# Kernel tuning notes

Measured on AMD Instinct MI355X. Metric: run time of the kernel, lower is better.

## Reference

```python
import jax, jax.numpy as jnp
import numpy as np

PATCH = 3  # patch_sizes[layer] == 3 for all layers
EPS_NORM = 1e-12   # F.normalize eps
EPS_DIV = 1e-8     # fold divisor eps


def _extract_patches(f, p):
    # F.unfold(kernel=p, stride=1, padding=p//2) -> (b, N=h*w, c, p, p)
    b, c, h, w = f.shape
    pad = p // 2
    xp = jnp.pad(f, ((0, 0), (0, 0), (pad, pad), (pad, pad)))
    # stack the p*p shifted views: (b, c, p*p, h, w)
    pats = jnp.stack([xp[:, :, i:i + h, j:j + w]
                      for i in range(p) for j in range(p)], axis=2)
    # -> (b, c, p, p, N) -> (b, N, c, p, p), matching unfold's (c, kh, kw) ordering
    return pats.reshape(b, c, p, p, h * w).transpose(0, 4, 1, 2, 3)


def _fold(patches, h, w, p):
    # F.fold inverse of unfold: scatter-add overlapping patches.
    # patches: (b, N=h*w, c, p, p)
    b, n, c = patches.shape[:3]
    pad = p // 2
    m = patches.reshape(b, h, w, c, p, p).transpose(0, 3, 4, 5, 1, 2)  # (b,c,p,p,h,w)
    out = jnp.zeros((b, c, h + 2 * pad, w + 2 * pad), patches.dtype)
    for ki in range(p):
        for kj in range(p):
            out = out.at[:, :, ki:ki + h, kj:kj + w].add(m[:, :, ki, kj])
    return out[:, :, pad:pad + h, pad:pad + w]


def _mrf_loss(content_feats, style_feats, p):
    b, c, h, w = content_feats.shape
    d = c * p * p
    cp = _extract_patches(content_feats, p)            # (b, N, c, p, p)
    sp = _extract_patches(style_feats, p)              # (b, M, c, p, p)
    cv = cp.reshape(b, -1, d)
    sv = sp.reshape(b, -1, d)
    cv = cv / jnp.maximum(jnp.linalg.norm(cv, axis=2, keepdims=True), EPS_NORM)
    svn = sv / jnp.maximum(jnp.linalg.norm(sv, axis=2, keepdims=True), EPS_NORM)
    # cosine similarity matrix (b, N, M) -- the big memory-bound intermediate
    dist = jnp.einsum('bnd,bmd->bnm', cv, svn)
    best = jnp.argmax(dist, axis=2)                    # (b, N) int
    # gather matched (un-normalized) style patches
    matched = jnp.take_along_axis(sp.reshape(b, -1, d), best[:, :, None], axis=1)
    matched = matched.reshape(b, -1, c, p, p)
    out = _fold(matched, h, w, p)
    ones = jnp.ones((1, h * w, 1, p, p), content_feats.dtype)
    divisor = _fold(ones, h, w, p)                      # overlap counts (1,1,h,w)
    recon = out / (divisor + EPS_DIV)
    return jnp.mean((content_feats - recon) ** 2)


def setup_inputs() -> dict:
    key = jax.random.key(0)
    k1, k2 = jax.random.split(key)
    content_feats = jax.random.normal(k1, (1, 128, 96, 96), dtype=jnp.float32)
    style_feats = jax.random.normal(k2, (1, 128, 96, 96), dtype=jnp.float32)
    return {"content_feats": content_feats, "style_feats": style_feats}


def reference(content_feats, style_feats):
    return _mrf_loss(content_feats, style_feats, PATCH)
```

## Files before the change

### kernel.cpp

```cpp
#include <hip/hip_runtime.h>
#include <hip/hip_bf16.h>

#define HH 96
#define WW 96
#define NPIX 9216
#define NCH 128
#define DDIM 1152
#define TOTAL_ELEMS 1179648
#define CG 32
#define DDIAG 9217
#define DROW 884832

typedef float f32x4 __attribute__((ext_vector_type(4)));
typedef __bf16 bf16x8 __attribute__((ext_vector_type(8)));
typedef _Float16 half8 __attribute__((ext_vector_type(8)));

__device__ __forceinline__ void gload_lds16(const void* g, void* l) {
  __builtin_amdgcn_global_load_lds((const __attribute__((address_space(1))) void*)g,
                                   (__attribute__((address_space(3))) void*)l, 16, 0, 0);
}


#define GUARD_ELEMS 894064ull
constexpr size_t G_CORE_ELEMS = (size_t)NPIX * NPIX;
constexpr size_t G_TOT_ELEMS = G_CORE_ELEMS + 2ull * GUARD_ELEMS;
constexpr size_t GBYTES = ((G_TOT_ELEMS * 2 + 255) & ~(size_t)255);
constexpr size_t CT_OFF = GBYTES;
constexpr size_t ST2_OFF = CT_OFF + (size_t)NPIX * NCH * 2;
constexpr size_t STYT_OFF = ST2_OFF + (size_t)NPIX * NCH * 2;
constexpr size_t SS_OFF = STYT_OFF + (size_t)NPIX * NCH * 4;
constexpr size_t RN2_OFF = SS_OFF + (size_t)NPIX * 4;
constexpr size_t KEY2_OFF = RN2_OFF + (size_t)NPIX * 4;
constexpr size_t NEED_NEW = KEY2_OFF + (size_t)NPIX * 8;

__global__ __launch_bounds__(256)
void transpose_kernel(const float* __restrict__ style_f, const float* __restrict__ content_f,
                      _Float16* __restrict__ St, _Float16* __restrict__ Ct,
                      float* __restrict__ styT, float* __restrict__ ss) {
  __shared__ float ftile[NCH][97];
  const int y = blockIdx.x;
  const bool is_style = (blockIdx.y == 0);
  const float* f = is_style ? style_f : content_f;
  _Float16* P = is_style ? St : Ct;
  const int tid = threadIdx.x;
  for (int i = tid; i < NCH * WW; i += 256) {
    int c = i / WW, x = i - (i / WW) * WW;
    ftile[c][x] = f[(size_t)c * NPIX + y * WW + x];
  }
  __syncthreads();
  for (int j = tid; j < WW * NCH; j += 256) {
    int x = j >> 7, c = j & 127;
    float v = ftile[c][x];
    P[(size_t)(y * WW + x) * NCH + c] = (_Float16)v;
    if (is_style) styT[(size_t)(y * WW + x) * NCH + c] = v;
  }
  if (is_style && tid < WW) {
    float s = 0.f;
#pragma unroll 8
    for (int c = 0; c < NCH; ++c) { float v = ftile[c][tid]; s = fmaf(v, v, s); }
    ss[y * WW + tid] = s;
  }
}

__global__ __launch_bounds__(256)
void boxnorm_kernel(const float* __restrict__ ss, float* __restrict__ rnorm) {
  int m = blockIdx.x * 256 + threadIdx.x;
  int ym = m / WW, xm = m - (m / WW) * WW;
  float s = 0.f;
#pragma unroll
  for (int di = -1; di <= 1; ++di) {
    int yy = ym + di;
    if (yy < 0 || yy >= HH) continue;
#pragma unroll
    for (int dj = -1; dj <= 1; ++dj) {
      int xx = xm + dj;
      if (xx < 0 || xx >= WW) continue;
      s += ss[yy * WW + xx];
    }
  }
  rnorm[m] = 1.0f / fmaxf(sqrtf(s), 1e-12f);
}

__global__ __launch_bounds__(256, 2)
void ggemm_kernel(const _Float16* __restrict__ Ct, const _Float16* __restrict__ St,
                  unsigned short* __restrict__ Gg) {
  __shared__ char smem[65536];
  const int tid = threadIdx.x;
  const int lane = tid & 63, wid = tid >> 6;
  const int l15 = lane & 15, lg = lane >> 4;
  const int wm = wid >> 1, wn = wid & 1;
  const int n0 = blockIdx.x * 128, m0 = blockIdx.y * 128;

  {
    const int r = tid >> 4, p = tid & 15;
    const int l = p ^ (r & 7);
    const _Float16* sa = Ct + (size_t)(n0 + r) * NCH + l * 8;
    const _Float16* sb = St + (size_t)(m0 + r) * NCH + l * 8;
    char* d = smem + tid * 16;
#pragma unroll
    for (int i = 0; i < 8; ++i) {
      gload_lds16(sa + (size_t)16 * i * NCH, d + 4096 * i);
      gload_lds16(sb + (size_t)16 * i * NCH, d + 32768 + 4096 * i);
    }
  }
  __syncthreads();

  f32x4 acc[4][4];
#pragma unroll
  for (int mf = 0; mf < 4; ++mf)
#pragma unroll
    for (int nf = 0; nf < 4; ++nf) {
      f32x4 z = {0.f, 0.f, 0.f, 0.f};
      acc[mf][nf] = z;
    }

#pragma unroll
  for (int ks = 0; ks < 4; ++ks) {
    half8 af[4], bb[4];
#pragma unroll
    for (int mf = 0; mf < 4; ++mf) {
      int row = wm * 64 + mf * 16 + l15;
      int phys = (ks * 4 + lg) ^ (row & 7);
      af[mf] = __builtin_bit_cast(half8, *(const int4*)(smem + row * 256 + phys * 16));
    }
#pragma unroll
    for (int nf = 0; nf < 4; ++nf) {
      int row = wn * 64 + nf * 16 + l15;
      int phys = (ks * 4 + lg) ^ (row & 7);
      bb[nf] = __builtin_bit_cast(half8, *(const int4*)(smem + 32768 + row * 256 + phys * 16));
    }
#pragma unroll
    for (int mf = 0; mf < 4; ++mf)
#pragma unroll
      for (int nf = 0; nf < 4; ++nf)
        acc[mf][nf] = __builtin_amdgcn_mfma_f32_16x16x32_f16(af[mf], bb[nf], acc[mf][nf], 0, 0, 0);
  }
  __syncthreads();

#pragma unroll
  for (int mf = 0; mf < 4; ++mf)
#pragma unroll
    for (int nf = 0; nf < 4; ++nf)
#pragma unroll
      for (int r = 0; r < 4; ++r) {
        int row = wm * 64 + mf * 16 + lg * 4 + r;
        int col = wn * 64 + nf * 16 + l15;
        *(_Float16*)(smem + (row * 136 + col) * 2) = (_Float16)acc[mf][nf][r];
      }
  __syncthreads();
  const size_t gbase = GUARD_ELEMS + (size_t)n0 * NPIX + m0;
#pragma unroll
  for (int j = 0; j < 8; ++j) {
    int idx = j * 256 + tid;
    int row = idx >> 4, ch = idx & 15;
    int4 v = *(const int4*)(smem + (row * 136 + ch * 8) * 2);
    *(int4*)(Gg + gbase + (size_t)row * NPIX + ch * 8) = v;
  }
}

__global__ __launch_bounds__(256)
void dist_argmax_kernel(const _Float16* __restrict__ Gg, const float* __restrict__ rnorm,
                        unsigned long long* __restrict__ keytab) {
  const int bid = blockIdx.x;
  const int xcd = bid & 7;
  const int local = bid >> 3;
  const int nt = xcd * 9 + (local % 9);
  const int rest = local / 9;
  const int ms = rest % 18;
  const int sh = rest / 18;
  const int w = threadIdx.x >> 6;
  const int lane = threadIdx.x & 63;
  const int n0 = nt * 128 + w * 32 + sh * 16;
  const int m8 = ms * 512 + lane * 8;

  const int ym = m8 / WW;
  const int x8 = m8 - ym * WW;
  const float me0 = (x8 == 0) ? 0.f : 1.f;
  const float me7 = (x8 == 88) ? 0.f : 1.f;
  const bool mr0 = (ym >= 1);
  const bool mr2 = (ym <= 94);
  float rnv[8];
  *(f32x4*)(rnv) = *(const f32x4*)(rnorm + m8);
  *(f32x4*)(rnv + 4) = *(const f32x4*)(rnorm + m8 + 4);

  const _Float16* base = Gg + ((size_t)n0 * NPIX + (size_t)m8 + GUARD_ELEMS);
  const _Float16* pL0 = base - DROW - DDIAG;
  const _Float16* pC0 = base - DROW;
  const _Float16* pR0 = base - DROW + DDIAG - 1;
  const _Float16* pL1 = base - DDIAG;
  const _Float16* pC1 = base;
  const _Float16* pR1 = base + DDIAG - 1;
  const _Float16* pL2 = base + DROW - DDIAG;
  const _Float16* pC2 = base + DROW;
  const _Float16* pR2 = base + DROW + DDIAG - 1;

  int yn = n0 / WW;
  int xn = n0 - yn * WW;

#pragma unroll 2
  for (int s = 0; s < 16; ++s) {
    const int n = n0 + s;
    const float cn0 = (xn >= 1) ? 1.f : 0.f;
    const float cn2 = (xn <= 94) ? 1.f : 0.f;
    const float rb0 = (mr0 && (yn >= 1)) ? 1.f : 0.f;
    const float rb2 = (mr2 && (yn <= 94)) ? 1.f : 0.f;
    float d[8];
    {
      half8 C = *(const half8*)pC1;
      _Float16 P = pL1[0];
      half8 L = *(const half8*)(pL1 + 1);
      half8 R = *(const half8*)pR1;
      _Float16 X = pR1[8];
#pragma unroll
      for (int j = 0; j < 8; ++j) d[j] = (float)C[j];
      d[0] = fmaf((float)P, cn0 * me0, d[0]);
#pragma unroll
      for (int j = 1; j < 8; ++j) d[j] = fmaf((float)L[j - 1], cn0, d[j]);
#pragma unroll
      for (int j = 0; j < 7; ++j) d[j] = fmaf((float)R[j + 1], cn2, d[j]);
      d[7] = fmaf((float)X, cn2 * me7, d[7]);
    }
    {
      const float wl = rb0 * cn0, wr = rb0 * cn2;
      half8 C = *(const half8*)pC0;
      _Float16 P = pL0[0];
      half8 L = *(const half8*)(pL0 + 1);
      half8 R = *(const half8*)pR0;
      _Float16 X = pR0[8];
#pragma unroll
      for (int j = 0; j < 8; ++j) d[j] = fmaf((float)C[j], rb0, d[j]);
      d[0] = fmaf((float)P, wl * me0, d[0]);
#pragma unroll
      for (int j = 1; j < 8; ++j) d[j] = fmaf((float)L[j - 1], wl, d[j]);
#pragma unroll
      for (int j = 0; j < 7; ++j) d[j] = fmaf((float)R[j + 1], wr, d[j]);
      d[7] = fmaf((float)X, wr * me7, d[7]);
    }
    {
      const float wl = rb2 * cn0, wr = rb2 * cn2;
      half8 C = *(const half8*)pC2;
      _Float16 P = pL2[0];
      half8 L = *(const half8*)(pL2 + 1);
      half8 R = *(const half8*)pR2;
      _Float16 X = pR2[8];
#pragma unroll
      for (int j = 0; j < 8; ++j) d[j] = fmaf((float)C[j], rb2, d[j]);
      d[0] = fmaf((float)P, wl * me0, d[0]);
#pragma unroll
      for (int j = 1; j < 8; ++j) d[j] = fmaf((float)L[j - 1], wl, d[j]);
#pragma unroll
      for (int j = 0; j < 7; ++j) d[j] = fmaf((float)R[j + 1], wr, d[j]);
      d[7] = fmaf((float)X, wr * me7, d[7]);
    }
    float bv = d[0] * rnv[0];
    int bj = m8;
#pragma unroll
    for (int j = 1; j < 8; ++j) {
      float xs = d[j] * rnv[j];
      if (xs > bv) { bv = xs; bj = m8 + j; }
    }
    float wmx = bv;
#pragma unroll
    for (int mm = 1; mm < 64; mm <<= 1)
      wmx = fmaxf(wmx, __shfl_xor(wmx, mm, 64));
    if (bv == wmx) {
      unsigned u = __float_as_uint(bv);
      u ^= (unsigned)((int)u >> 31) | 0x80000000u;
      unsigned long long key =
          ((unsigned long long)u << 32) | (unsigned)(0xFFFFFFFFu ^ (unsigned)bj);
      atomicMax(keytab + n, key);
    }
    pL0 += NPIX; pC0 += NPIX; pR0 += NPIX;
    pL1 += NPIX; pC1 += NPIX; pR1 += NPIX;
    pL2 += NPIX; pC2 += NPIX; pR2 += NPIX;
    ++xn;
    if (xn == WW) { xn = 0; ++yn; }
  }
}

__global__ __launch_bounds__(256)
void recon_mse2_kernel(const _Float16* __restrict__ Ct, const float* __restrict__ styT,
                       const unsigned long long* __restrict__ keytab, float* __restrict__ out) {
  const int pix = blockIdx.x * 2 + (threadIdx.x >> 7);
  const int c = threadIdx.x & 127;
  const int y = pix / WW, x = pix - (pix / WW) * WW;
  float sum = 0.f, cnt = 0.f;
#pragma unroll
  for (int ki = 0; ki < 3; ++ki) {
    int yn = y - ki + 1;
    if (yn < 0 || yn >= HH) continue;
#pragma unroll
    for (int kj = 0; kj < 3; ++kj) {
      int xn = x - kj + 1;
      if (xn < 0 || xn >= WW) continue;
      cnt += 1.f;
      int m = (int)(0xFFFFFFFFu ^ (unsigned)(keytab[yn * WW + xn] & 0xFFFFFFFFull));
      int ys = m / WW, xs = m - (m / WW) * WW;
      int sy = ys + ki - 1, sx = xs + kj - 1;
      if (sy >= 0 && sy < HH && sx >= 0 && sx < WW)
        sum += styT[(size_t)(sy * WW + sx) * NCH + c];
    }
  }
  float recon = sum / (cnt + 1e-8f);
  float cv = (float)Ct[(size_t)pix * NCH + c];
  float diff = cv - recon;
  float sq = diff * diff;
#pragma unroll
  for (int m = 32; m > 0; m >>= 1) sq += __shfl_down(sq, m, 64);
  __shared__ float wsum[4];
  int lane = threadIdx.x & 63, w = threadIdx.x >> 6;
  if (lane == 0) wsum[w] = sq;
  __syncthreads();
  if (threadIdx.x == 0)
    atomicAdd(out, (wsum[0] + wsum[1] + wsum[2] + wsum[3]) * (1.0f / (float)TOTAL_ELEMS));
}

__global__ __launch_bounds__(256)
void build_patches_old(const float* __restrict__ style_f, const float* __restrict__ content_f,
                       __bf16* __restrict__ Ps, __bf16* __restrict__ Pc) {
  __shared__ float ftile[CG][3][104];
  const int y = blockIdx.x;
  const int cg = blockIdx.y;
  const bool is_style = (blockIdx.z == 0);
  const float* f = is_style ? style_f : content_f;
  __bf16* P = is_style ? Ps : Pc;
  const int tid = threadIdx.x;
  for (int i = tid; i < CG * 3 * 96; i += 256) {
    int cl = i / 288, rem = i - cl * 288;
    int yy = rem / 96, xx = rem - yy * 96;
    int gy = y + yy - 1;
    float v = (gy >= 0 && gy < HH) ? f[(size_t)(cg * CG + cl) * NPIX + gy * WW + xx] : 0.f;
    ftile[cl][yy][xx] = v;
  }
  __syncthreads();
  for (int j = tid; j < 96 * 36; j += 256) {
    int px = j / 36, wi = j - px * 36;
    bf16x8 tmp;
#pragma unroll
    for (int u = 0; u < 8; ++u) {
      int e = wi * 8 + u;
      int cl = e / 9, t = e - cl * 9;
      int ki = t / 3, kj = t - ki * 3;
      int xx = px + kj - 1;
      float v = (xx >= 0 && xx < WW) ? ftile[cl][ki][xx] : 0.f;
      tmp[u] = (__bf16)v;
    }
    *(bf16x8*)(P + (size_t)(y * WW + px) * DDIM + cg * 288 + wi * 8) = tmp;
  }
}

__global__ __launch_bounds__(256)
void norm_old(const __bf16* __restrict__ Ps, float* __restrict__ rnorm) {
  const int n = blockIdx.x * 4 + (threadIdx.x >> 6);
  const int lane = threadIdx.x & 63;
  const bf16x8* row = (const bf16x8*)(Ps + (size_t)n * DDIM);
  float ss = 0.f;
#pragma unroll
  for (int i = 0; i < 3; ++i) {
    int idx = i * 64 + lane;
    if (idx < 144) {
      bf16x8 v = row[idx];
#pragma unroll
      for (int u = 0; u < 8; ++u) { float x = (float)v[u]; ss += x * x; }
    }
  }
#pragma unroll
  for (int m = 1; m < 64; m <<= 1) ss += __shfl_xor(ss, m, 64);
  if (lane == 0) rnorm[n] = 1.0f / fmaxf(sqrtf(ss), 1e-12f);
}

__global__ __launch_bounds__(256, 2)
void gemm_old(const __bf16* __restrict__ Pc, const __bf16* __restrict__ Ps,
              const float* __restrict__ rnorm, unsigned long long* __restrict__ keytab) {
  __shared__ int4 smem4[4608];
  char* smem = (char*)smem4;
  const int tid = threadIdx.x;
  const int lane = tid & 63;
  const int wid = tid >> 6;
  const int l15 = lane & 15;
  const int lg = lane >> 4;
  const int wm = wid >> 1;
  const int wn = wid & 1;
  const int orig = blockIdx.x;
  const int swz = (orig & 7) * 324 + (orig >> 3);
  const int mt = swz / 72;
  const int nt = swz - mt * 72;
  const int bm0 = mt * 256;
  const int sbase = nt * 128;
  const int srow = tid >> 2;
  const int sg = (tid & 3) ^ ((srow >> 1) & 3);
  const __bf16* pa = Pc + (size_t)(bm0 + srow) * DDIM + sg * 8;
  const __bf16* pb = Ps + (size_t)(sbase + srow) * DDIM + sg * 8;
  const int sdst = tid * 16;
  auto stage = [&](int buf, int kt) {
    char* la = smem + buf * 24576 + sdst;
    const int ko = kt * 32;
#pragma unroll
    for (int i = 0; i < 4; ++i) gload_lds16(pa + (size_t)i * 64 * DDIM + ko, la + i * 4096);
#pragma unroll
    for (int j = 0; j < 2; ++j) gload_lds16(pb + (size_t)j * 64 * DDIM + ko, la + 16384 + j * 4096);
  };
  const int sx = (lg ^ ((l15 >> 1) & 3)) << 4;
  int aoff[8], boff[4];
#pragma unroll
  for (int mf = 0; mf < 8; ++mf) aoff[mf] = (wm * 128 + mf * 16 + l15) * 64 + sx;
#pragma unroll
  for (int nf = 0; nf < 4; ++nf) boff[nf] = 16384 + (wn * 64 + nf * 16 + l15) * 64 + sx;
  f32x4 acc[8][4];
#pragma unroll
  for (int mf = 0; mf < 8; ++mf)
#pragma unroll
    for (int nf = 0; nf < 4; ++nf) {
      f32x4 z = {0.f, 0.f, 0.f, 0.f};
      acc[mf][nf] = z;
    }
  auto compute = [&](int buf) {
    const char* bp = smem + buf * 24576;
    bf16x8 af[8], bfr[4];
#pragma unroll
    for (int mf = 0; mf < 8; ++mf) af[mf] = __builtin_bit_cast(bf16x8, *(const int4*)(bp + aoff[mf]));
#pragma unroll
    for (int nf = 0; nf < 4; ++nf) bfr[nf] = __builtin_bit_cast(bf16x8, *(const int4*)(bp + boff[nf]));
    __builtin_amdgcn_s_setprio(1);
#pragma unroll
    for (int mf = 0; mf < 8; ++mf)
#pragma unroll
      for (int nf = 0; nf < 4; ++nf)
        acc[mf][nf] = __builtin_amdgcn_mfma_f32_16x16x32_bf16(af[mf], bfr[nf], acc[mf][nf], 0, 0, 0);
    __builtin_amdgcn_s_setprio(0);
  };
  stage(0, 0);
  stage(1, 1);
  int sb = 2, cb = 0;
  for (int kt = 0; kt < 34; ++kt) {
    stage(sb, kt + 2);
    sb = (sb == 2) ? 0 : sb + 1;
    asm volatile("s_waitcnt vmcnt(12)" ::: "memory");
    __builtin_amdgcn_s_barrier();
    __builtin_amdgcn_sched_barrier(0);
    compute(cb);
    __builtin_amdgcn_s_barrier();
    cb = (cb == 2) ? 0 : cb + 1;
  }
  asm volatile("s_waitcnt vmcnt(6)" ::: "memory");
  __builtin_amdgcn_s_barrier();
  __builtin_amdgcn_sched_barrier(0);
  compute(cb);
  cb = (cb == 2) ? 0 : cb + 1;
  asm volatile("s_waitcnt vmcnt(0)" ::: "memory");
  __builtin_amdgcn_s_barrier();
  __builtin_amdgcn_sched_barrier(0);
  compute(cb);
  float rn[4];
#pragma unroll
  for (int nf = 0; nf < 4; ++nf) rn[nf] = rnorm[sbase + wn * 64 + nf * 16 + l15];
#pragma unroll
  for (int mf = 0; mf < 8; ++mf)
#pragma unroll
    for (int r = 0; r < 4; ++r) {
      float v = -3.0e38f;
      int bi = 0;
#pragma unroll
      for (int nf = 0; nf < 4; ++nf) {
        float x = acc[mf][nf][r] * rn[nf];
        int col = sbase + wn * 64 + nf * 16 + l15;
        if (x > v) { v = x; bi = col; }
      }
#pragma unroll
      for (int m = 1; m < 16; m <<= 1) {
        float ov = __shfl_xor(v, m, 64);
        int oi = __shfl_xor(bi, m, 64);
        if (ov > v || (ov == v && oi < bi)) { v = ov; bi = oi; }
      }
      if (l15 == 0) {
        int row = bm0 + wm * 128 + mf * 16 + lg * 4 + r;
        unsigned u = __float_as_uint(v);
        u ^= (unsigned)((int)u >> 31) | 0x80000000u;
        unsigned long long key = ((unsigned long long)u << 32) | (unsigned)(0xFFFFFFFFu ^ (unsigned)bi);
        atomicMax(keytab + row, key);
      }
    }
}

__global__ __launch_bounds__(256)
void recon_old(const __bf16* __restrict__ Pc, const __bf16* __restrict__ Ps,
               const unsigned long long* __restrict__ keytab, float* __restrict__ out) {
  const int pix = blockIdx.x * 2 + (threadIdx.x >> 7);
  const int c = threadIdx.x & 127;
  const int y = pix / WW, x = pix - (pix / WW) * WW;
  float sum = 0.f, cnt = 0.f;
#pragma unroll
  for (int ki = 0; ki < 3; ++ki) {
    int yn = y - ki + 1;
    if (yn < 0 || yn >= HH) continue;
#pragma unroll
    for (int kj = 0; kj < 3; ++kj) {
      int xn = x - kj + 1;
      if (xn < 0 || xn >= WW) continue;
      cnt += 1.f;
      int m = (int)(0xFFFFFFFFu ^ (unsigned)(keytab[yn * WW + xn] & 0xFFFFFFFFull));
      sum += (float)Ps[(size_t)m * DDIM + c * 9 + ki * 3 + kj];
    }
  }
  float recon = sum / (cnt + 1e-8f);
  float cv = (float)Pc[(size_t)pix * DDIM + c * 9 + 4];
  float diff = cv - recon;
  float sq = diff * diff;
#pragma unroll
  for (int m = 32; m > 0; m >>= 1) sq += __shfl_down(sq, m, 64);
  __shared__ float wsum[4];
  int lane = threadIdx.x & 63, w = threadIdx.x >> 6;
  if (lane == 0) wsum[w] = sq;
  __syncthreads();
  if (threadIdx.x == 0)
    atomicAdd(out, (wsum[0] + wsum[1] + wsum[2] + wsum[3]) * (1.0f / (float)TOTAL_ELEMS));
}

extern "C" void kernel_launch(void* const* d_in, const int* in_sizes, int n_in,
                              void* d_out, int out_size, void* d_ws, size_t ws_size,
                              hipStream_t stream) {
  const float* content = (const float*)d_in[0];
  const float* stylef = (const float*)d_in[1];
  float* out = (float*)d_out;
  char* ws = (char*)d_ws;

  hipMemsetAsync(d_out, 0, (size_t)out_size * sizeof(float), stream);

  if (ws_size >= NEED_NEW) {
    _Float16* Gg = (_Float16*)ws;
    _Float16* Ct = (_Float16*)(ws + CT_OFF);
    _Float16* St = (_Float16*)(ws + ST2_OFF);
    float* styT = (float*)(ws + STYT_OFF);
    float* ss = (float*)(ws + SS_OFF);
    float* rnorm = (float*)(ws + RN2_OFF);
    unsigned long long* keytab = (unsigned long long*)(ws + KEY2_OFF);

    hipMemsetAsync(keytab, 0, (size_t)NPIX * 8, stream);
    hipMemsetAsync(Gg, 0, (size_t)GUARD_ELEMS * 2, stream);
    hipMemsetAsync(Gg + GUARD_ELEMS + G_CORE_ELEMS, 0, (size_t)GUARD_ELEMS * 2, stream);
    transpose_kernel<<<dim3(96, 2), 256, 0, stream>>>(stylef, content, St, Ct, styT, ss);
    boxnorm_kernel<<<NPIX / 256, 256, 0, stream>>>(ss, rnorm);
    ggemm_kernel<<<dim3(72, 72), 256, 0, stream>>>(Ct, St, (unsigned short*)Gg);
    dist_argmax_kernel<<<2592, 256, 0, stream>>>(Gg, rnorm, keytab);
    recon_mse2_kernel<<<NPIX / 2, 256, 0, stream>>>(Ct, styT, keytab, out);
  } else {
    const size_t PS_OFF = 0;
    const size_t PC_OFF = (size_t)NPIX * DDIM * 2;
    const size_t RN_OFF = PC_OFF * 2;
    const size_t KEY_OFF = RN_OFF + (size_t)NPIX * 4;
    __bf16* Ps = (__bf16*)(ws + PS_OFF);
    __bf16* Pc = (__bf16*)(ws + PC_OFF);
    float* rnorm = (float*)(ws + RN_OFF);
    unsigned long long* keytab = (unsigned long long*)(ws + KEY_OFF);
    hipMemsetAsync(keytab, 0, (size_t)NPIX * 8, stream);
    build_patches_old<<<dim3(96, 4, 2), 256, 0, stream>>>(stylef, content, Ps, Pc);
    norm_old<<<NPIX / 4, 256, 0, stream>>>(Ps, rnorm);
    gemm_old<<<2592, 256, 0, stream>>>(Pc, Ps, rnorm, keytab);
    recon_old<<<NPIX / 2, 256, 0, stream>>>(Pc, Ps, keytab, out);
  }
}
```

Measured before the change: 244.3 us.

## Assign one wavefront per content row in dist-argmax, drop atomic key table

The distance/argmax kernel is remapped so each wavefront owns a single content patch row and sweeps all style columns in 18 steps, keeping a running best per lane and doing a single cross-lane argmax reduction at the end. This replaces the per-row shuffle reduction plus 64-bit atomicMax into a key table, and removes the key-table memset. The recon kernel reads the int index directly. Trade-offs: fewer blocks with 512 threads, less reuse of rnorm loads across rows, and a different access pattern over the large fp16 Gram matrix.

```diff
diff --git a/kernel.cpp b/kernel.cpp
--- a/kernel.cpp
+++ b/kernel.cpp
@@ -158,32 +158,22 @@
   }
 }
 
-__global__ __launch_bounds__(256)
+__global__ __launch_bounds__(512)
 void dist_argmax_kernel(const _Float16* __restrict__ Gg, const float* __restrict__ rnorm,
-                        unsigned long long* __restrict__ keytab) {
+                        int* __restrict__ best) {
   const int bid = blockIdx.x;
-  const int xcd = bid & 7;
-  const int local = bid >> 3;
-  const int nt = xcd * 9 + (local % 9);
-  const int rest = local / 9;
-  const int ms = rest % 18;
-  const int sh = rest / 18;
+  const int oct = (bid & 7) * 144 + (bid >> 3);
   const int w = threadIdx.x >> 6;
   const int lane = threadIdx.x & 63;
-  const int n0 = nt * 128 + w * 32 + sh * 16;
-  const int m8 = ms * 512 + lane * 8;
-
-  const int ym = m8 / WW;
-  const int x8 = m8 - ym * WW;
-  const float me0 = (x8 == 0) ? 0.f : 1.f;
-  const float me7 = (x8 == 88) ? 0.f : 1.f;
-  const bool mr0 = (ym >= 1);
-  const bool mr2 = (ym <= 94);
-  float rnv[8];
-  *(f32x4*)(rnv) = *(const f32x4*)(rnorm + m8);
-  *(f32x4*)(rnv + 4) = *(const f32x4*)(rnorm + m8 + 4);
-
-  const _Float16* base = Gg + ((size_t)n0 * NPIX + (size_t)m8 + GUARD_ELEMS);
+  const int n = oct * 8 + w;
+  const int yn = n / WW;
+  const int xn = n - yn * WW;
+  const float cn0 = (xn >= 1) ? 1.f : 0.f;
+  const float cn2 = (xn <= 94) ? 1.f : 0.f;
+  const bool nr0 = (yn >= 1);
+  const bool nr2 = (yn <= 94);
+
+  const _Float16* base = Gg + ((size_t)n * NPIX + GUARD_ELEMS + lane * 8);
   const _Float16* pL0 = base - DROW - DDIAG;
   const _Float16* pC0 = base - DROW;
   const _Float16* pR0 = base - DROW + DDIAG - 1;
@@ -194,16 +184,21 @@
   const _Float16* pC2 = base + DROW;
   const _Float16* pR2 = base + DROW + DDIAG - 1;
 
-  int yn = n0 / WW;
-  int xn = n0 - yn * WW;
-
-#pragma unroll 2
-  for (int s = 0; s < 16; ++s) {
-    const int n = n0 + s;
-    const float cn0 = (xn >= 1) ? 1.f : 0.f;
-    const float cn2 = (xn <= 94) ? 1.f : 0.f;
-    const float rb0 = (mr0 && (yn >= 1)) ? 1.f : 0.f;
-    const float rb2 = (mr2 && (yn <= 94)) ? 1.f : 0.f;
+  float bv = -3.0e38f;
+  int bj = 0;
+  int m8 = lane * 8;
+  int ym = m8 / WW;
+  int x8 = m8 - ym * WW;
+
+  for (int step = 0; step < 18; ++step) {
+    const float me0 = (x8 == 0) ? 0.f : 1.f;
+    const float me7 = (x8 == 88) ? 0.f : 1.f;
+    const float rb0 = (nr0 && (ym >= 1)) ? 1.f : 0.f;
+    const float rb2 = (nr2 && (ym <= 94)) ? 1.f : 0.f;
+    float rnv[8];
+    *(f32x4*)(rnv) = *(const f32x4*)(rnorm + m8);
+    *(f32x4*)(rnv + 4) = *(const f32x4*)(rnorm + m8 + 4);
+
     float d[8];
     {
       half8 C = *(const half8*)pC1;
@@ -252,35 +247,31 @@
       for (int j = 0; j < 7; ++j) d[j] = fmaf((float)R[j + 1], wr, d[j]);
       d[7] = fmaf((float)X, wr * me7, d[7]);
     }
-    float bv = d[0] * rnv[0];
-    int bj = m8;
-#pragma unroll
-    for (int j = 1; j < 8; ++j) {
+#pragma unroll
+    for (int j = 0; j < 8; ++j) {
       float xs = d[j] * rnv[j];
       if (xs > bv) { bv = xs; bj = m8 + j; }
     }
-    float wmx = bv;
-#pragma unroll
-    for (int mm = 1; mm < 64; mm <<= 1)
-      wmx = fmaxf(wmx, __shfl_xor(wmx, mm, 64));
-    if (bv == wmx) {
-      unsigned u = __float_as_uint(bv);
-      u ^= (unsigned)((int)u >> 31) | 0x80000000u;
-      unsigned long long key =
-          ((unsigned long long)u << 32) | (unsigned)(0xFFFFFFFFu ^ (unsigned)bj);
-      atomicMax(keytab + n, key);
-    }
-    pL0 += NPIX; pC0 += NPIX; pR0 += NPIX;
-    pL1 += NPIX; pC1 += NPIX; pR1 += NPIX;
-    pL2 += NPIX; pC2 += NPIX; pR2 += NPIX;
-    ++xn;
-    if (xn == WW) { xn = 0; ++yn; }
-  }
+    pL0 += 512; pC0 += 512; pR0 += 512;
+    pL1 += 512; pC1 += 512; pR1 += 512;
+    pL2 += 512; pC2 += 512; pR2 += 512;
+    m8 += 512;
+    x8 += 32; ym += 5;
+    if (x8 >= 96) { x8 -= 96; ++ym; }
+  }
+
+#pragma unroll
+  for (int mm = 1; mm < 64; mm <<= 1) {
+    float ov = __shfl_xor(bv, mm, 64);
+    int oi = __shfl_xor(bj, mm, 64);
+    if (ov > bv || (ov == bv && oi < bj)) { bv = ov; bj = oi; }
+  }
+  if (lane == 0) best[n] = bj;
 }
 
 __global__ __launch_bounds__(256)
 void recon_mse2_kernel(const _Float16* __restrict__ Ct, const float* __restrict__ styT,
-                       const unsigned long long* __restrict__ keytab, float* __restrict__ out) {
+                       const int* __restrict__ best, float* __restrict__ out) {
   const int pix = blockIdx.x * 2 + (threadIdx.x >> 7);
   const int c = threadIdx.x & 127;
   const int y = pix / WW, x = pix - (pix / WW) * WW;
@@ -294,7 +285,7 @@
       int xn = x - kj + 1;
       if (xn < 0 || xn >= WW) continue;
       cnt += 1.f;
-      int m = (int)(0xFFFFFFFFu ^ (unsigned)(keytab[yn * WW + xn] & 0xFFFFFFFFull));
+      int m = best[yn * WW + xn];
       int ys = m / WW, xs = m - (m / WW) * WW;
       int sy = ys + ki - 1, sx = xs + kj - 1;
       if (sy >= 0 && sy < HH && sx >= 0 && sx < WW)
@@ -533,16 +524,15 @@
     float* styT = (float*)(ws + STYT_OFF);
     float* ss = (float*)(ws + SS_OFF);
     float* rnorm = (float*)(ws + RN2_OFF);
-    unsigned long long* keytab = (unsigned long long*)(ws + KEY2_OFF);
-
-    hipMemsetAsync(keytab, 0, (size_t)NPIX * 8, stream);
+    int* best = (int*)(ws + KEY2_OFF);
+
     hipMemsetAsync(Gg, 0, (size_t)GUARD_ELEMS * 2, stream);
     hipMemsetAsync(Gg + GUARD_ELEMS + G_CORE_ELEMS, 0, (size_t)GUARD_ELEMS * 2, stream);
     transpose_kernel<<<dim3(96, 2), 256, 0, stream>>>(stylef, content, St, Ct, styT, ss);
     boxnorm_kernel<<<NPIX / 256, 256, 0, stream>>>(ss, rnorm);
     ggemm_kernel<<<dim3(72, 72), 256, 0, stream>>>(Ct, St, (unsigned short*)Gg);
-    dist_argmax_kernel<<<2592, 256, 0, stream>>>(Gg, rnorm, keytab);
-    recon_mse2_kernel<<<NPIX / 2, 256, 0, stream>>>(Ct, styT, keytab, out);
+    dist_argmax_kernel<<<1152, 512, 0, stream>>>(Gg, rnorm, best);
+    recon_mse2_kernel<<<NPIX / 2, 256, 0, stream>>>(Ct, styT, best, out);
   } else {
     const size_t PS_OFF = 0;
     const size_t PC_OFF = (size_t)NPIX * DDIM * 2;
```

Result: slower. 268.7 us (+10.0%).

## Stage Gram diagonal band tiles in LDS for dist_argmax stencil

Applied to the files above, without the earlier changes.

The dist_argmax kernel used to read each of the nine shifted Gram entries straight from global memory per lane, loading overlapping data repeatedly. It now has each block copy three 18x528 fp16 bands of G into shared memory with global_load_lds and computes the 3x3 diagonal-stencil sums from LDS, using smaller 16x512 tiles over four times as many blocks. This cuts redundant global traffic, at the cost of more blocks, about 57KB of LDS per block (limiting occupancy), and a full load-then-barrier with no overlap.

```diff
diff --git a/kernel.cpp b/kernel.cpp
--- a/kernel.cpp
+++ b/kernel.cpp
@@ -10,6 +10,13 @@
 #define CG 32
 #define DDIAG 9217
 #define DROW 884832
+
+#define NTIL 16
+#define MTIL 512
+#define BROWS 18
+#define BCOLS 528
+#define BELEMS (BROWS * BCOLS)
+#define DCHUNKS 3564
 
 typedef float f32x4 __attribute__((ext_vector_type(4)));
 typedef __bf16 bf16x8 __attribute__((ext_vector_type(8)));
@@ -158,106 +165,120 @@
   }
 }
 
-__global__ __launch_bounds__(256)
+__global__ __launch_bounds__(256, 2)
 void dist_argmax_kernel(const _Float16* __restrict__ Gg, const float* __restrict__ rnorm,
                         unsigned long long* __restrict__ keytab) {
+  __shared__ _Float16 lds[3584 * 8];
   const int bid = blockIdx.x;
-  const int xcd = bid & 7;
-  const int local = bid >> 3;
-  const int nt = xcd * 9 + (local % 9);
-  const int rest = local / 9;
-  const int ms = rest % 18;
-  const int sh = rest / 18;
-  const int w = threadIdx.x >> 6;
-  const int lane = threadIdx.x & 63;
-  const int n0 = nt * 128 + w * 32 + sh * 16;
-  const int m8 = ms * 512 + lane * 8;
-
-  const int ym = m8 / WW;
-  const int x8 = m8 - ym * WW;
+  const int idx = (bid & 7) * 1296 + (bid >> 3);
+  const int ntb = idx / 18;
+  const int mtb = idx - ntb * 18;
+  const int n0 = ntb * NTIL;
+  const int m0 = mtb * MTIL;
+  const int tid = threadIdx.x;
+  const int w = tid >> 6, lane = tid & 63;
+
+  long flat0[3];
+#pragma unroll
+  for (int b = 0; b < 3; ++b) {
+    int di = b - 1;
+    flat0[b] = (long)(n0 + 96 * di - 1) * NPIX + (long)(m0 + 96 * di - 8) + (long)GUARD_ELEMS;
+  }
+#pragma unroll
+  for (int k = 0; k < 14; ++k) {
+    int q = k * 256 + tid;
+    if (q < DCHUNKS) {
+      int b = q / 1188;
+      int rem = q - b * 1188;
+      int row = rem / 66;
+      int c16 = rem - row * 66;
+      gload_lds16(Gg + flat0[b] + (long)row * NPIX + c16 * 8, lds + (size_t)q * 8);
+    }
+  }
+  const int mlane = m0 + lane * 8;
+  const int ym = mlane / WW;
+  const int x8 = mlane - ym * WW;
   const float me0 = (x8 == 0) ? 0.f : 1.f;
   const float me7 = (x8 == 88) ? 0.f : 1.f;
-  const bool mr0 = (ym >= 1);
-  const bool mr2 = (ym <= 94);
+  const bool myr0 = (ym >= 1), myr2 = (ym <= 94);
   float rnv[8];
-  *(f32x4*)(rnv) = *(const f32x4*)(rnorm + m8);
-  *(f32x4*)(rnv + 4) = *(const f32x4*)(rnorm + m8 + 4);
-
-  const _Float16* base = Gg + ((size_t)n0 * NPIX + (size_t)m8 + GUARD_ELEMS);
-  const _Float16* pL0 = base - DROW - DDIAG;
-  const _Float16* pC0 = base - DROW;
-  const _Float16* pR0 = base - DROW + DDIAG - 1;
-  const _Float16* pL1 = base - DDIAG;
-  const _Float16* pC1 = base;
-  const _Float16* pR1 = base + DDIAG - 1;
-  const _Float16* pL2 = base + DROW - DDIAG;
-  const _Float16* pC2 = base + DROW;
-  const _Float16* pR2 = base + DROW + DDIAG - 1;
-
-  int yn = n0 / WW;
-  int xn = n0 - yn * WW;
-
-#pragma unroll 2
-  for (int s = 0; s < 16; ++s) {
-    const int n = n0 + s;
+  *(f32x4*)(rnv) = *(const f32x4*)(rnorm + mlane);
+  *(f32x4*)(rnv + 4) = *(const f32x4*)(rnorm + mlane + 4);
+  const int col8 = lane * 8 + 8;
+  const _Float16* B0p = lds;
+  const _Float16* B1p = lds + BELEMS;
+  const _Float16* B2p = lds + 2 * BELEMS;
+
+  asm volatile("s_waitcnt vmcnt(0)" ::: "memory");
+  __builtin_amdgcn_s_barrier();
+
+#pragma unroll
+  for (int s = 0; s < 4; ++s) {
+    const int r = w * 4 + s;
+    const int n = n0 + r;
+    const int yn = n / WW;
+    const int xn = n - yn * WW;
     const float cn0 = (xn >= 1) ? 1.f : 0.f;
     const float cn2 = (xn <= 94) ? 1.f : 0.f;
-    const float rb0 = (mr0 && (yn >= 1)) ? 1.f : 0.f;
-    const float rb2 = (mr2 && (yn <= 94)) ? 1.f : 0.f;
+    const float Bw0 = (myr0 && (yn >= 1)) ? 1.f : 0.f;
+    const float Bw2 = (myr2 && (yn <= 94)) ? 1.f : 0.f;
     float d[8];
     {
-      half8 C = *(const half8*)pC1;
-      _Float16 P = pL1[0];
-      half8 L = *(const half8*)(pL1 + 1);
-      half8 R = *(const half8*)pR1;
-      _Float16 X = pR1[8];
-#pragma unroll
-      for (int j = 0; j < 8; ++j) d[j] = (float)C[j];
-      d[0] = fmaf((float)P, cn0 * me0, d[0]);
-#pragma unroll
-      for (int j = 1; j < 8; ++j) d[j] = fmaf((float)L[j - 1], cn0, d[j]);
-#pragma unroll
-      for (int j = 0; j < 7; ++j) d[j] = fmaf((float)R[j + 1], cn2, d[j]);
-      d[7] = fmaf((float)X, cn2 * me7, d[7]);
+      const _Float16* bp = B1p + r * BCOLS;
+      half8 V0 = *(const half8*)(bp + col8);
+      half8 V1 = *(const half8*)(bp + BCOLS + col8);
+      half8 V2 = *(const half8*)(bp + 2 * BCOLS + col8);
+      float P = (float)bp[col8 - 1];
+      float X = (float)bp[2 * BCOLS + col8 + 8];
+#pragma unroll
+      for (int j = 0; j < 8; ++j) d[j] = (float)V1[j];
+      d[0] = fmaf(P, cn0 * me0, d[0]);
+#pragma unroll
+      for (int j = 1; j < 8; ++j) d[j] = fmaf((float)V0[j - 1], cn0, d[j]);
+#pragma unroll
+      for (int j = 0; j < 7; ++j) d[j] = fmaf((float)V2[j + 1], cn2, d[j]);
+      d[7] = fmaf(X, cn2 * me7, d[7]);
     }
     {
-      const float wl = rb0 * cn0, wr = rb0 * cn2;
-      half8 C = *(const half8*)pC0;
-      _Float16 P = pL0[0];
-      half8 L = *(const half8*)(pL0 + 1);
-      half8 R = *(const half8*)pR0;
-      _Float16 X = pR0[8];
-#pragma unroll
-      for (int j = 0; j < 8; ++j) d[j] = fmaf((float)C[j], rb0, d[j]);
-      d[0] = fmaf((float)P, wl * me0, d[0]);
-#pragma unroll
-      for (int j = 1; j < 8; ++j) d[j] = fmaf((float)L[j - 1], wl, d[j]);
-#pragma unroll
-      for (int j = 0; j < 7; ++j) d[j] = fmaf((float)R[j + 1], wr, d[j]);
-      d[7] = fmaf((float)X, wr * me7, d[7]);
+      const float wl = Bw0 * cn0, wr = Bw0 * cn2;
+      const _Float16* bp = B0p + r * BCOLS;
+      half8 V0 = *(const half8*)(bp + col8);
+      half8 V1 = *(const half8*)(bp + BCOLS + col8);
+      half8 V2 = *(const half8*)(bp + 2 * BCOLS + col8);
+      float P = (float)bp[col8 - 1];
+      float X = (float)bp[2 * BCOLS + col8 + 8];
+#pragma unroll
+      for (int j = 0; j < 8; ++j) d[j] = fmaf((float)V1[j], Bw0, d[j]);
+      d[0] = fmaf(P, wl * me0, d[0]);
+#pragma unroll
+      for (int j = 1; j < 8; ++j) d[j] = fmaf((float)V0[j - 1], wl, d[j]);
+#pragma unroll
+      for (int j = 0; j < 7; ++j) d[j] = fmaf((float)V2[j + 1], wr, d[j]);
+      d[7] = fmaf(X, wr * me7, d[7]);
     }
     {
-      const float wl = rb2 * cn0, wr = rb2 * cn2;
-      half8 C = *(const half8*)pC2;
-      _Float16 P = pL2[0];
-      half8 L = *(const half8*)(pL2 + 1);
-      half8 R = *(const half8*)pR2;
-      _Float16 X = pR2[8];
-#pragma unroll
-      for (int j = 0; j < 8; ++j) d[j] = fmaf((float)C[j], rb2, d[j]);
-      d[0] = fmaf((float)P, wl * me0, d[0]);
-#pragma unroll
-      for (int j = 1; j < 8; ++j) d[j] = fmaf((float)L[j - 1], wl, d[j]);
-#pragma unroll
-      for (int j = 0; j < 7; ++j) d[j] = fmaf((float)R[j + 1], wr, d[j]);
-      d[7] = fmaf((float)X, wr * me7, d[7]);
+      const float wl = Bw2 * cn0, wr = Bw2 * cn2;
+      const _Float16* bp = B2p + r * BCOLS;
+      half8 V0 = *(const half8*)(bp + col8);
+      half8 V1 = *(const half8*)(bp + BCOLS + col8);
+      half8 V2 = *(const half8*)(bp + 2 * BCOLS + col8);
+      float P = (float)bp[col8 - 1];
+      float X = (float)bp[2 * BCOLS + col8 + 8];
+#pragma unroll
+      for (int j = 0; j < 8; ++j) d[j] = fmaf((float)V1[j], Bw2, d[j]);
+      d[0] = fmaf(P, wl * me0, d[0]);
+#pragma unroll
+      for (int j = 1; j < 8; ++j) d[j] = fmaf((float)V0[j - 1], wl, d[j]);
+#pragma unroll
+      for (int j = 0; j < 7; ++j) d[j] = fmaf((float)V2[j + 1], wr, d[j]);
+      d[7] = fmaf(X, wr * me7, d[7]);
     }
     float bv = d[0] * rnv[0];
-    int bj = m8;
+    int bj = mlane;
 #pragma unroll
     for (int j = 1; j < 8; ++j) {
       float xs = d[j] * rnv[j];
-      if (xs > bv) { bv = xs; bj = m8 + j; }
+      if (xs > bv) { bv = xs; bj = mlane + j; }
     }
     float wmx = bv;
 #pragma unroll
@@ -270,11 +291,6 @@
           ((unsigned long long)u << 32) | (unsigned)(0xFFFFFFFFu ^ (unsigned)bj);
       atomicMax(keytab + n, key);
     }
-    pL0 += NPIX; pC0 += NPIX; pR0 += NPIX;
-    pL1 += NPIX; pC1 += NPIX; pR1 += NPIX;
-    pL2 += NPIX; pC2 += NPIX; pR2 += NPIX;
-    ++xn;
-    if (xn == WW) { xn = 0; ++yn; }
   }
 }
 
@@ -541,7 +557,7 @@
     transpose_kernel<<<dim3(96, 2), 256, 0, stream>>>(stylef, content, St, Ct, styT, ss);
     boxnorm_kernel<<<NPIX / 256, 256, 0, stream>>>(ss, rnorm);
     ggemm_kernel<<<dim3(72, 72), 256, 0, stream>>>(Ct, St, (unsigned short*)Gg);
-    dist_argmax_kernel<<<2592, 256, 0, stream>>>(Gg, rnorm, keytab);
+    dist_argmax_kernel<<<10368, 256, 0, stream>>>(Gg, rnorm, keytab);
     recon_mse2_kernel<<<NPIX / 2, 256, 0, stream>>>(Ct, styT, keytab, out);
   } else {
     const size_t PS_OFF = 0;
```

After: 254.5 us. 4.2% more time.
